# Optimization experiments

Hardware: AMD Instinct MI355X
Metric: run time of the kernel (lower is better)

## Reference

```python
import jax, jax.numpy as jnp
import numpy as np

EMBED = 1024
HEAD = 64
B, S = 4, 4096

def setup_inputs() -> dict:
    key = jax.random.key(0)
    k1, k2, k3, k4, k5, k6 = jax.random.split(key, 6)
    scale = 1.0 / np.sqrt(EMBED)
    return {
        "query": jax.random.normal(k1, (B, S, EMBED), dtype=jnp.float32),
        "key": jax.random.normal(k2, (B, S, EMBED), dtype=jnp.float32),
        "value": jax.random.normal(k3, (B, S, EMBED), dtype=jnp.float32),
        "wq": jax.random.normal(k4, (EMBED, HEAD), dtype=jnp.float32) * scale,
        "wk": jax.random.normal(k5, (EMBED, HEAD), dtype=jnp.float32) * scale,
        "wv": jax.random.normal(k6, (EMBED, HEAD), dtype=jnp.float32) * scale,
    }

def reference(query, key, value, wq, wk, wv):
    # projections (bias-free linears)
    q = query @ wq            # [B,S,H]
    k = key @ wk              # [B,S,H]
    v = value @ wv            # [B,S,H]
    scores = jnp.einsum('bqh,bkh->bqk', q, k) / jnp.sqrt(jnp.float32(HEAD))
    S_len = scores.shape[-1]
    causal = jnp.tril(jnp.ones((S_len, S_len), dtype=bool))
    scores = jnp.where(causal, scores, -jnp.inf)
    attn = jax.nn.softmax(scores, axis=-1)
    return attn @ v           # [B,S,H]
```

## Files before the change

### kernel.cpp

```cpp
#include <hip/hip_runtime.h>
#include <hip/hip_bf16.h>

#define EMBED 1024
#define HEAD 64
#define SEQ 4096

typedef __attribute__((ext_vector_type(8))) short short8;
typedef __attribute__((ext_vector_type(4))) float f32x4;

union S8u { short8 v; uint u[4]; ushort s[8]; };
union U4f { uint4 q; float f[4]; };

__device__ __forceinline__ ushort f2bf(float f) {
  union { float f; uint u; } x; x.f = f;
  return (ushort)((x.u + 0x7fffu + ((x.u >> 16) & 1u)) >> 16);
}

__device__ __forceinline__ ushort f2bf_n(float f) {
  union { __hip_bfloat16 h; ushort u; } cv;
  cv.h = __float2bfloat16(f);
  return cv.u;
}

__device__ __forceinline__ short8 ld16(const ushort* p) {
  uint4 q = *(const uint4*)p;
  S8u t; t.u[0] = q.x; t.u[1] = q.y; t.u[2] = q.z; t.u[3] = q.w;
  return t.v;
}

__device__ __forceinline__ void glds16(const void* g, void* l) {
  __builtin_amdgcn_global_load_lds((const __attribute__((address_space(1))) void*)g,
                                   (__attribute__((address_space(3))) void*)l, 16, 0, 0);
}

__global__ __launch_bounds__(256) void prep_w(const float* __restrict__ wq,
                                              const float* __restrict__ wk,
                                              const float* __restrict__ wv,
                                              ushort* __restrict__ wT) {
  int idx = blockIdx.x * 256 + threadIdx.x;
  if (idx >= 3 * HEAD * EMBED) return;
  int t = idx >> 16;
  int rem = idx & 0xFFFF;
  int c = rem >> 10;
  int k = rem & 1023;
  const float* w = (t == 0) ? wq : (t == 1) ? wk : wv;
  wT[idx] = f2bf_n(w[k * HEAD + c]);
}

__global__ __launch_bounds__(256, 3) void proj_kernel(
    const float* __restrict__ qsrc, const float* __restrict__ ksrc,
    const float* __restrict__ vsrc, const ushort* __restrict__ wT,
    ushort* __restrict__ qb, ushort* __restrict__ kb, ushort* __restrict__ vt) {
  __shared__ __align__(16) char smem[49152];

  const int t = blockIdx.y;
  const float* src = (t == 0) ? qsrc : (t == 1) ? ksrc : vsrc;
  const ushort* wt = wT + t * (HEAD * EMBED);
  const int tid = threadIdx.x;
  const int lane = tid & 63;
  const int wid = tid >> 6;
  const int c = lane & 15;
  const int g = lane >> 4;
  const int row0 = blockIdx.x * 64;
  const int phase = (blockIdx.x + 5 * blockIdx.y) & 15;

  const char* gA[4];
#pragma unroll
  for (int mm = 0; mm < 4; ++mm) {
    int r = mm * 16 + wid * 4 + (lane >> 4);
    gA[mm] = (const char*)(src + (size_t)(row0 + r) * EMBED) +
             ((((lane & 15) * 16)) ^ ((r & 7) << 4));
  }
  const char* gB[2];
#pragma unroll
  for (int m2 = 0; m2 < 2; ++m2) {
    int r2 = m2 * 32 + wid * 8 + (lane >> 3);
    gB[m2] = (const char*)(wt + (size_t)r2 * EMBED) +
             ((((lane & 7) * 16)) ^ ((r2 & 7) << 4));
  }

  const int rA = (wid * 16 + c) * 256;
  const int swc = (c & 7) << 4;

  f32x4 acc[4];
#pragma unroll
  for (int i = 0; i < 4; ++i) acc[i] = {0.f, 0.f, 0.f, 0.f};

#define STAGE(CUR, KIDX)                                                          \
  do {                                                                            \
    _Pragma("unroll") for (int mm = 0; mm < 4; ++mm)                              \
      glds16(gA[mm] + (KIDX) * 256, smem + (CUR) * 16384 + mm * 4096 + wid * 1024); \
    _Pragma("unroll") for (int m2 = 0; m2 < 2; ++m2)                              \
      glds16(gB[m2] + (KIDX) * 128, smem + 32768 + (CUR) * 8192 + m2 * 4096 + wid * 1024); \
  } while (0)

  STAGE(0, phase);

  for (int r = 0; r < 16; ++r) {
    if (r + 1 < 16) {
      STAGE((r + 1) & 1, (r + 1 + phase) & 15);
      asm volatile("s_waitcnt vmcnt(6)" ::: "memory");
    } else {
      asm volatile("s_waitcnt vmcnt(0)" ::: "memory");
    }
    __builtin_amdgcn_s_barrier();
    asm volatile("" ::: "memory");

    const int cur = r & 1;
    const char* bufA = smem + cur * 16384;
    const char* bufB = smem + 32768 + cur * 8192;
#pragma unroll
    for (int s = 0; s < 2; ++s) {
      U4f af0, af1;
      af0.q = *(const uint4*)(bufA + rA + ((128 * s + 32 * g) ^ swc));
      af1.q = *(const uint4*)(bufA + rA + ((128 * s + 32 * g + 16) ^ swc));
      S8u a;
      a.s[0] = f2bf_n(af0.f[0]); a.s[1] = f2bf_n(af0.f[1]);
      a.s[2] = f2bf_n(af0.f[2]); a.s[3] = f2bf_n(af0.f[3]);
      a.s[4] = f2bf_n(af1.f[0]); a.s[5] = f2bf_n(af1.f[1]);
      a.s[6] = f2bf_n(af1.f[2]); a.s[7] = f2bf_n(af1.f[3]);
#pragma unroll
      for (int nf = 0; nf < 4; ++nf) {
        uint4 bq = *(const uint4*)(bufB + (16 * nf + c) * 128 + ((64 * s + 16 * g) ^ swc));
        S8u b; b.u[0] = bq.x; b.u[1] = bq.y; b.u[2] = bq.z; b.u[3] = bq.w;
        acc[nf] = __builtin_amdgcn_mfma_f32_16x16x32_bf16(a.v, b.v, acc[nf], 0, 0, 0);
      }
    }
    asm volatile("" ::: "memory");
    __builtin_amdgcn_s_barrier();
  }
#undef STAGE

  __syncthreads();
  if (t == 2) {
    ushort (*vtile)[72] = (ushort(*)[72])smem;
#pragma unroll
    for (int nf = 0; nf < 4; ++nf)
#pragma unroll
      for (int rr = 0; rr < 4; ++rr)
        vtile[nf * 16 + c][wid * 16 + 4 * g + rr] = f2bf_n(acc[nf][rr]);
    __syncthreads();
    int d = tid >> 2;
    int s0 = (tid & 3) << 4;
    int bb = row0 >> 12;
    int sbase = row0 & (SEQ - 1);
    ushort* dst = vt + ((size_t)(bb * HEAD + d) << 12) + sbase + s0;
    const uint4* srcp = (const uint4*)&vtile[d][s0];
    *(uint4*)dst = srcp[0];
    *(uint4*)(dst + 8) = srcp[1];
  } else {
    int row_base = row0 + wid * 16 + 4 * g;
    float scale = (t == 0) ? 0.18033688011112042f : 1.0f;
    ushort* dstb = (t == 0) ? qb : kb;
#pragma unroll
    for (int nf = 0; nf < 4; ++nf)
#pragma unroll
      for (int rr = 0; rr < 4; ++rr)
        dstb[(size_t)(row_base + rr) * HEAD + nf * 16 + c] = f2bf_n(acc[nf][rr] * scale);
  }
}

__global__ __launch_bounds__(512, 2) void flash_kernel(
    const ushort* __restrict__ qb, const ushort* __restrict__ kb,
    const ushort* __restrict__ vt, float* __restrict__ Opart,
    float* __restrict__ mlpart) {
  __shared__ __align__(16) char smem[16384];

  const int tid = threadIdx.x;
  const int lane = tid & 63;
  const int w = tid >> 6;
  const int c = lane & 15, g = lane >> 4;

  const int bid = blockIdx.x;
  const int band = 15 - (bid >> 4);
  const int b = (bid >> 2) & 3;
  const int j = bid & 3;
  const int ck = band + 1;
  const int kt0 = j * ck;
  const int q0w = band * 256 + w * 32;

  const int srow = tid >> 3;
  const int scol = (tid & 7) << 4;
  const int sdst = srow * 128 + (scol ^ ((srow & 7) << 4));
  const char* kgp = (const char*)(kb + (size_t)b * SEQ * HEAD) + (size_t)kt0 * 8192 + tid * 16;
  const char* vgp = (const char*)(vt + (size_t)b * HEAD * SEQ) + (size_t)srow * 8192 + kt0 * 128 + scol;

  short8 qa[2][2];
#pragma unroll
  for (int qf = 0; qf < 2; ++qf) {
    const ushort* qrow = qb + (size_t)(b * SEQ + q0w + 16 * qf + c) * HEAD + 8 * g;
    qa[qf][0] = ld16(qrow);
    qa[qf][1] = ld16(qrow + 32);
  }

  f32x4 O[4][2];
#pragma unroll
  for (int i = 0; i < 4; ++i)
#pragma unroll
    for (int qf = 0; qf < 2; ++qf) O[i][qf] = {0.f, 0.f, 0.f, 0.f};
  float m[2] = {-1e30f, -1e30f};
  float l[2] = {0.f, 0.f};

  uint4 sK = *(const uint4*)kgp;
  uint4 sV = *(const uint4*)vgp;

  for (int r = 0; r < ck; ++r) {
    *(uint4*)(smem + sdst) = sK;
    *(uint4*)(smem + 8192 + sdst) = sV;
    __syncthreads();

    if (r + 1 < ck) {
      kgp += 8192; vgp += 128;
      sK = *(const uint4*)kgp;
      sV = *(const uint4*)vgp;
    }

    const int kt = kt0 + r;
    const int k0 = kt << 6;
    if (k0 <= q0w + 31) {
      f32x4 Sf[4][2];
#pragma unroll
      for (int i = 0; i < 4; ++i)
#pragma unroll
        for (int qf = 0; qf < 2; ++qf) Sf[i][qf] = {0.f, 0.f, 0.f, 0.f};
#pragma unroll
      for (int nf = 0; nf < 4; ++nf) {
        int row = 16 * nf + c;
        int sw = (row & 7) << 4;
        uint4 kv = *(const uint4*)(smem + row * 128 + ((16 * g) ^ sw));
        S8u ka0;
        ka0.u[0] = kv.x; ka0.u[1] = kv.y; ka0.u[2] = kv.z; ka0.u[3] = kv.w;
#pragma unroll
        for (int qf = 0; qf < 2; ++qf)
          Sf[nf][qf] = __builtin_amdgcn_mfma_f32_16x16x32_bf16(ka0.v, qa[qf][0], Sf[nf][qf], 0, 0, 0);
        uint4 kv2 = *(const uint4*)(smem + row * 128 + ((64 + 16 * g) ^ sw));
        S8u ka1;
        ka1.u[0] = kv2.x; ka1.u[1] = kv2.y; ka1.u[2] = kv2.z; ka1.u[3] = kv2.w;
#pragma unroll
        for (int qf = 0; qf < 2; ++qf)
          Sf[nf][qf] = __builtin_amdgcn_mfma_f32_16x16x32_bf16(ka1.v, qa[qf][1], Sf[nf][qf], 0, 0, 0);
      }

      if (k0 + 63 > q0w) {
#pragma unroll
        for (int nf = 0; nf < 4; ++nf)
#pragma unroll
          for (int qf = 0; qf < 2; ++qf)
#pragma unroll
            for (int rr = 0; rr < 4; ++rr)
              if (k0 + nf * 16 + 4 * g + rr > q0w + 16 * qf + c) Sf[nf][qf][rr] = -1e30f;
      }

#pragma unroll
      for (int qf = 0; qf < 2; ++qf) {
        float x0 = fmaxf(fmaxf(Sf[0][qf][0], Sf[0][qf][1]), fmaxf(Sf[0][qf][2], Sf[0][qf][3]));
        float x1 = fmaxf(fmaxf(Sf[1][qf][0], Sf[1][qf][1]), fmaxf(Sf[1][qf][2], Sf[1][qf][3]));
        float x2 = fmaxf(fmaxf(Sf[2][qf][0], Sf[2][qf][1]), fmaxf(Sf[2][qf][2], Sf[2][qf][3]));
        float x3 = fmaxf(fmaxf(Sf[3][qf][0], Sf[3][qf][1]), fmaxf(Sf[3][qf][2], Sf[3][qf][3]));
        float rm = fmaxf(fmaxf(x0, x1), fmaxf(x2, x3));
        rm = fmaxf(rm, __shfl_xor(rm, 16));
        rm = fmaxf(rm, __shfl_xor(rm, 32));
        rm = fmaxf(rm, m[qf]);
        float alpha = exp2f(m[qf] - rm);
        m[qf] = rm;
#pragma unroll
        for (int nf = 0; nf < 4; ++nf)
#pragma unroll
          for (int rr = 0; rr < 4; ++rr)
            Sf[nf][qf][rr] = exp2f(Sf[nf][qf][rr] - rm);
        float s0 = (Sf[0][qf][0] + Sf[0][qf][1]) + (Sf[0][qf][2] + Sf[0][qf][3]);
        float s1 = (Sf[1][qf][0] + Sf[1][qf][1]) + (Sf[1][qf][2] + Sf[1][qf][3]);
        float s2 = (Sf[2][qf][0] + Sf[2][qf][1]) + (Sf[2][qf][2] + Sf[2][qf][3]);
        float s3 = (Sf[3][qf][0] + Sf[3][qf][1]) + (Sf[3][qf][2] + Sf[3][qf][3]);
        float rs = (s0 + s1) + (s2 + s3);
        rs += __shfl_xor(rs, 16);
        rs += __shfl_xor(rs, 32);
        l[qf] = l[qf] * alpha + rs;
#pragma unroll
        for (int nf = 0; nf < 4; ++nf)
#pragma unroll
          for (int rr = 0; rr < 4; ++rr)
            O[nf][qf][rr] *= alpha;

#pragma unroll
        for (int sl = 0; sl < 2; ++sl) {
          S8u pa;
#pragma unroll
          for (int rr = 0; rr < 4; ++rr) {
            pa.s[rr]     = f2bf(Sf[2 * sl][qf][rr]);
            pa.s[rr + 4] = f2bf(Sf[2 * sl + 1][qf][rr]);
          }
#pragma unroll
          for (int nf = 0; nf < 4; ++nf) {
            int row = 16 * nf + c;
            int sw = (row & 7) << 4;
            S8u vbf;
            uint2 lo = *(const uint2*)(smem + 8192 + row * 128 + ((64 * sl + 8 * g) ^ sw));
            uint2 hi = *(const uint2*)(smem + 8192 + row * 128 + ((64 * sl + 32 + 8 * g) ^ sw));
            vbf.u[0] = lo.x; vbf.u[1] = lo.y; vbf.u[2] = hi.x; vbf.u[3] = hi.y;
            O[nf][qf] = __builtin_amdgcn_mfma_f32_16x16x32_bf16(vbf.v, pa.v, O[nf][qf], 0, 0, 0);
          }
        }
      }
    }
    __syncthreads();
  }

  const size_t pi = (size_t)((b * 16 + band) * 4 + j);
#pragma unroll
  for (int qf = 0; qf < 2; ++qf) {
    int ql = w * 32 + 16 * qf + c;
#pragma unroll
    for (int nf = 0; nf < 4; ++nf)
      *(f32x4*)&Opart[pi * 16384 + (size_t)ql * 64 + 16 * nf + 4 * g] = O[nf][qf];
    if (g == 0) {
      mlpart[pi * 512 + ql * 2]     = m[qf];
      mlpart[pi * 512 + ql * 2 + 1] = l[qf];
    }
  }
}

__global__ __launch_bounds__(256) void merge_kernel(const float* __restrict__ Opart,
                                                    const float* __restrict__ mlpart,
                                                    float* __restrict__ out) {
  int i = blockIdx.x * 256 + threadIdx.x;
  int dq = i & 15;
  int row = i >> 4;
  int b = row >> 12;
  int qrow = row & 4095;
  int band = qrow >> 8;
  int q = qrow & 255;
  size_t pi0 = (size_t)((b * 16 + band) * 4);

  float mm[4], M = -1e30f;
#pragma unroll
  for (int jj = 0; jj < 4; ++jj) { mm[jj] = mlpart[(pi0 + jj) * 512 + q * 2]; M = fmaxf(M, mm[jj]); }
  float wgt[4], L = 0.f;
#pragma unroll
  for (int jj = 0; jj < 4; ++jj) {
    wgt[jj] = exp2f(mm[jj] - M);
    L += wgt[jj] * mlpart[(pi0 + jj) * 512 + q * 2 + 1];
  }
  f32x4 acc = {0.f, 0.f, 0.f, 0.f};
#pragma unroll
  for (int jj = 0; jj < 4; ++jj) {
    f32x4 t = *(const f32x4*)&Opart[(pi0 + jj) * 16384 + (size_t)q * 64 + 4 * dq];
#pragma unroll
    for (int rr = 0; rr < 4; ++rr) acc[rr] += wgt[jj] * t[rr];
  }
  float inv = 1.0f / L;
  f32x4 res;
#pragma unroll
  for (int rr = 0; rr < 4; ++rr) res[rr] = acc[rr] * inv;
  *(f32x4*)&out[(size_t)row * HEAD + 4 * dq] = res;
}

extern "C" void kernel_launch(void* const* d_in, const int* in_sizes, int n_in,
                              void* d_out, int out_size, void* d_ws, size_t ws_size,
                              hipStream_t stream) {
  const float* qsrc = (const float*)d_in[0];
  const float* ksrc = (const float*)d_in[1];
  const float* vsrc = (const float*)d_in[2];
  const float* wq = (const float*)d_in[3];
  const float* wk = (const float*)d_in[4];
  const float* wv = (const float*)d_in[5];
  float* out = (float*)d_out;

  char* ws = (char*)d_ws;
  ushort* wT = (ushort*)ws;
  ushort* qb = (ushort*)(ws + 393216);
  ushort* kb = (ushort*)(ws + 393216 + 2097152);
  ushort* vt = (ushort*)(ws + 393216 + 2 * 2097152);
  float* Opart = (float*)(ws + 393216 + 3 * 2097152);
  float* mlpart = (float*)(ws + 393216 + 3 * 2097152 + 16777216);

  prep_w<<<dim3(768), dim3(256), 0, stream>>>(wq, wk, wv, wT);
  proj_kernel<<<dim3(256, 3), dim3(256), 0, stream>>>(qsrc, ksrc, vsrc, wT, qb, kb, vt);
  flash_kernel<<<dim3(256), dim3(512), 0, stream>>>(qb, kb, vt, Opart, mlpart);
  merge_kernel<<<dim3(1024), dim3(256), 0, stream>>>(Opart, mlpart, out);
}
```

Measured before the change: 88.39 us.

## Stage only activations in LDS with larger K tiles, read weights from global

The projection kernel now stages only the fp32 activation tile through LDS, using 128-wide K chunks over 8 iterations instead of 64-wide chunks over 16. The bf16 weight fragments are loaded straight from global memory, expected to hit in cache, rather than being staged in shared memory. The aim is fewer barriers and pipeline steps and more bytes in flight per stage. In exchange LDS use grows to 64KB, occupancy drops from 3 to 2 blocks per CU, and weight loads become global-latency reads inside the MFMA loop.

```diff
diff --git a/kernel.cpp b/kernel.cpp
--- a/kernel.cpp
+++ b/kernel.cpp
@@ -47,11 +47,11 @@
   wT[idx] = f2bf_n(w[k * HEAD + c]);
 }
 
-__global__ __launch_bounds__(256, 3) void proj_kernel(
+__global__ __launch_bounds__(256, 2) void proj_kernel(
     const float* __restrict__ qsrc, const float* __restrict__ ksrc,
     const float* __restrict__ vsrc, const ushort* __restrict__ wT,
     ushort* __restrict__ qb, ushort* __restrict__ kb, ushort* __restrict__ vt) {
-  __shared__ __align__(16) char smem[49152];
+  __shared__ __align__(16) char smem[65536];
 
   const int t = blockIdx.y;
   const float* src = (t == 0) ? qsrc : (t == 1) ? ksrc : vsrc;
@@ -62,58 +62,51 @@
   const int c = lane & 15;
   const int g = lane >> 4;
   const int row0 = blockIdx.x * 64;
-  const int phase = (blockIdx.x + 5 * blockIdx.y) & 15;
-
-  const char* gA[4];
+  const int phase = (blockIdx.x + 5 * blockIdx.y) & 7;
+
+  const int srow = lane >> 5;
+  const char* baseC[4];
 #pragma unroll
   for (int mm = 0; mm < 4; ++mm) {
-    int r = mm * 16 + wid * 4 + (lane >> 4);
-    gA[mm] = (const char*)(src + (size_t)(row0 + r) * EMBED) +
-             ((((lane & 15) * 16)) ^ ((r & 7) << 4));
-  }
-  const char* gB[2];
-#pragma unroll
-  for (int m2 = 0; m2 < 2; ++m2) {
-    int r2 = m2 * 32 + wid * 8 + (lane >> 3);
-    gB[m2] = (const char*)(wt + (size_t)r2 * EMBED) +
-             ((((lane & 7) * 16)) ^ ((r2 & 7) << 4));
-  }
-
-  const int rA = (wid * 16 + c) * 256;
-  const int swc = (c & 7) << 4;
+    int rr = 2 * mm + srow;
+    baseC[mm] = (const char*)(src + (size_t)(row0 + 16 * wid + rr) * EMBED) +
+                (((lane & 31) * 16) ^ ((rr & 7) << 4));
+  }
+
+  const int sw = (c & 7) << 4;
+  const int rAbase = (wid * 16 + c) * 512;
 
   f32x4 acc[4];
 #pragma unroll
   for (int i = 0; i < 4; ++i) acc[i] = {0.f, 0.f, 0.f, 0.f};
 
-#define STAGE(CUR, KIDX)                                                          \
-  do {                                                                            \
-    _Pragma("unroll") for (int mm = 0; mm < 4; ++mm)                              \
-      glds16(gA[mm] + (KIDX) * 256, smem + (CUR) * 16384 + mm * 4096 + wid * 1024); \
-    _Pragma("unroll") for (int m2 = 0; m2 < 2; ++m2)                              \
-      glds16(gB[m2] + (KIDX) * 128, smem + 32768 + (CUR) * 8192 + m2 * 4096 + wid * 1024); \
+#define STAGE(CUR, KI)                                                         \
+  do {                                                                         \
+    const size_t kbyte = (size_t)(KI) * 512;                                   \
+    _Pragma("unroll") for (int j = 0; j < 8; ++j)                              \
+      glds16(baseC[j & 3] + (j >> 2) * 32768 + kbyte,                          \
+             smem + (CUR) * 32768 + wid * 8192 + j * 1024);                    \
   } while (0)
 
   STAGE(0, phase);
 
-  for (int r = 0; r < 16; ++r) {
-    if (r + 1 < 16) {
-      STAGE((r + 1) & 1, (r + 1 + phase) & 15);
-      asm volatile("s_waitcnt vmcnt(6)" ::: "memory");
+  for (int r = 0; r < 8; ++r) {
+    if (r + 1 < 8) {
+      STAGE((r + 1) & 1, (r + 1 + phase) & 7);
+      asm volatile("s_waitcnt vmcnt(8)" ::: "memory");
     } else {
       asm volatile("s_waitcnt vmcnt(0)" ::: "memory");
     }
     __builtin_amdgcn_s_barrier();
     asm volatile("" ::: "memory");
 
-    const int cur = r & 1;
-    const char* bufA = smem + cur * 16384;
-    const char* bufB = smem + 32768 + cur * 8192;
-#pragma unroll
-    for (int s = 0; s < 2; ++s) {
+    const char* bufA = smem + (r & 1) * 32768;
+    const int kelem = ((r + phase) & 7) * 128;
+#pragma unroll
+    for (int s = 0; s < 4; ++s) {
       U4f af0, af1;
-      af0.q = *(const uint4*)(bufA + rA + ((128 * s + 32 * g) ^ swc));
-      af1.q = *(const uint4*)(bufA + rA + ((128 * s + 32 * g + 16) ^ swc));
+      af0.q = *(const uint4*)(bufA + rAbase + ((s * 128 + 32 * g) ^ sw));
+      af1.q = *(const uint4*)(bufA + rAbase + ((s * 128 + 32 * g + 16) ^ sw));
       S8u a;
       a.s[0] = f2bf_n(af0.f[0]); a.s[1] = f2bf_n(af0.f[1]);
       a.s[2] = f2bf_n(af0.f[2]); a.s[3] = f2bf_n(af0.f[3]);
@@ -121,9 +114,8 @@
       a.s[6] = f2bf_n(af1.f[2]); a.s[7] = f2bf_n(af1.f[3]);
 #pragma unroll
       for (int nf = 0; nf < 4; ++nf) {
-        uint4 bq = *(const uint4*)(bufB + (16 * nf + c) * 128 + ((64 * s + 16 * g) ^ swc));
-        S8u b; b.u[0] = bq.x; b.u[1] = bq.y; b.u[2] = bq.z; b.u[3] = bq.w;
-        acc[nf] = __builtin_amdgcn_mfma_f32_16x16x32_bf16(a.v, b.v, acc[nf], 0, 0, 0);
+        short8 b = ld16(wt + (size_t)(nf * 16 + c) * EMBED + kelem + s * 32 + 8 * g);
+        acc[nf] = __builtin_amdgcn_mfma_f32_16x16x32_bf16(a.v, b, acc[nf], 0, 0, 0);
       }
     }
     asm volatile("" ::: "memory");
```

New measurement: 118.4 us. +34.0%, slower.
